# Optimization experiments

Hardware: AMD Instinct MI355X
Metric: run time of the kernel (lower is better)

Reference implementation:

```python
import jax, jax.numpy as jnp
import numpy as np

BATCH, SEQLEN, D_MODEL, D_STATE = 2, 2048, 512, 64
DT_MIN, DT_MAX = 1e-4, 1e-3


def setup_inputs() -> dict:
    key = jax.random.key(0)
    k1, k2, k3, k4 = jax.random.split(key, 4)
    u = jax.random.normal(k1, (BATCH, SEQLEN, D_MODEL), dtype=jnp.float32)
    # real parts of the complex params B, C (imag parts never affect the output)
    B_re = (jax.random.normal(k2, (D_STATE,), dtype=jnp.float32) / np.float32(np.sqrt(D_STATE)))
    C_re = (jax.random.normal(k3, (D_STATE,), dtype=jnp.float32) / np.float32(np.sqrt(D_STATE)))
    log_dt = jax.random.uniform(k4, (D_MODEL,), minval=np.log(DT_MIN), maxval=np.log(DT_MAX)).astype(jnp.float32)
    D = jnp.ones((D_MODEL,), dtype=jnp.float32)
    return {"u": u, "B_re": B_re, "C_re": C_re, "log_dt": log_dt, "D": D}


def reference(u, B_re, C_re, log_dt, D):
    # u: [B, L, H]; B_re/C_re: [N]; log_dt/D: [H]
    N = B_re.shape[0]
    # buffer: log_A = -0.5 * log(1 + n/N), n = 1..N  (A = exp(log_A) in (0,1])
    log_A = -0.5 * jnp.log1p(jnp.arange(1, N + 1, dtype=jnp.float32) / N)
    A = jnp.exp(log_A)                       # [N]
    delta = jnp.exp(log_dt)                  # [H]
    A_d = jnp.exp(delta[:, None] * A[None, :])          # [H, N]
    B_d = (A_d - 1.0) * B_re[None, :] * delta[:, None]  # [H, N]

    Bsz, L, H = u.shape
    x0 = jnp.zeros((Bsz, H, N), dtype=u.dtype)

    def step(x, u_t):                        # x: [B,H,N], u_t: [B,H]
        x = A_d * x + B_d * u_t[..., None]
        y_t = jnp.einsum('bhn,n->bh', x, C_re) + D * u_t
        return x, y_t

    _, ys = jax.lax.scan(step, x0, jnp.swapaxes(u, 0, 1))  # ys: [L,B,H]
    return jnp.swapaxes(ys, 0, 1)                          # [B,L,H]
```

## Files before the change

kernel.cpp:

```cpp
#include <hip/hip_runtime.h>
#include <math.h>


#define BATCH   2
#define SEQLEN  2048
#define DMODEL  512
#define DSTATE  64
#define T_CHUNK 32
#define NCHUNK  64
#define RT      8

__device__ __forceinline__ float A_cont(int n) {
    return rsqrtf(1.0f + (float)(n + 1) * (1.0f / 64.0f));
}

__global__ __launch_bounds__(256) void k_xlocal(const float* __restrict__ u,
                                                const float* __restrict__ B_re,
                                                const float* __restrict__ log_dt,
                                                float* __restrict__ xl) {
    int bid = (int)blockIdx.x;
    int wb  = (bid & 7) * 128 + (bid >> 3);
    int tid = wb * 256 + (int)threadIdx.x;
    int h  = tid & (DMODEL - 1);
    int ng = (tid >> 9) & 3;
    int c  = (tid >> 11) & (NCHUNK - 1);
    int b  = tid >> 17;
    float delta = expf(log_dt[h]);
    float Ad[16], Bd[16], x[16];
    #pragma unroll
    for (int nn = 0; nn < 16; ++nn) {
        int n = ng * 16 + nn;
        float dA = delta * A_cont(n);
        Ad[nn] = expf(dA);
        Bd[nn] = expm1f(dA) * B_re[n] * delta;
        x[nn] = 0.0f;
    }
    const float* up = u + ((size_t)(b * SEQLEN + c * T_CHUNK)) * DMODEL + h;
    #pragma unroll 8
    for (int s = 0; s < T_CHUNK; ++s) {
        float uv = up[(size_t)s * DMODEL];
        #pragma unroll
        for (int nn = 0; nn < 16; ++nn)
            x[nn] = fmaf(Ad[nn], x[nn], Bd[nn] * uv);
    }
    float* xp = xl + ((size_t)((b * NCHUNK + c) * DSTATE + ng * 16)) * DMODEL + h;
    #pragma unroll
    for (int nn = 0; nn < 16; ++nn) xp[(size_t)nn * DMODEL] = x[nn];
}

__global__ __launch_bounds__(256) void k_scanset(const float* __restrict__ B_re,
                                                 const float* __restrict__ C_re,
                                                 const float* __restrict__ log_dt,
                                                 const float* __restrict__ Dp,
                                                 float* __restrict__ xl,
                                                 float* __restrict__ Kbuf,
                                                 float* __restrict__ AdTab,
                                                 float* __restrict__ CpStep) {
    int tid = blockIdx.x * 256 + threadIdx.x;
    {
        int h = tid & (DMODEL - 1);
        int n = (tid >> 9) & (DSTATE - 1);
        int b = tid >> 15;
        float delta = expf(log_dt[h]);
        float ApT = expf(delta * A_cont(n) * (float)T_CHUNK);
        float* base = xl + ((size_t)(b * NCHUNK * DSTATE + n)) * DMODEL + h;
        float v[NCHUNK - 1];
        #pragma unroll
        for (int c = 0; c < NCHUNK - 1; ++c)
            v[c] = base[(size_t)c * DSTATE * DMODEL];
        float s = 0.0f;
        #pragma unroll
        for (int c = 0; c < NCHUNK - 1; ++c) { s = fmaf(ApT, s, v[c]); v[c] = s; }
        #pragma unroll
        for (int c = 0; c < NCHUNK - 1; ++c)
            base[(size_t)c * DSTATE * DMODEL] = v[c];
    }
    if (tid < 32768) {
        int h = tid & (DMODEL - 1);
        int n = tid >> 9;
        float delta = expf(log_dt[h]);
        float Adn = expf(delta * A_cont(n));
        AdTab[n * DMODEL + h] = Adn;
        float sq = Adn * Adn; sq = sq * sq;
        float e8 = sq * sq;
        float p = C_re[n] * Adn;
        #pragma unroll
        for (int i = 0; i < 4; ++i) {
            CpStep[(i * DSTATE + n) * DMODEL + h] = p;
            p *= e8;
        }
        if (n < T_CHUNK) {
            int j = n;
            float acc = (j == 0) ? Dp[h] : 0.0f;
            for (int nn = 0; nn < DSTATE; ++nn) {
                float dAn = delta * A_cont(nn);
                float Bdv = expm1f(dAn) * B_re[nn] * delta;
                acc = fmaf(C_re[nn] * Bdv, expf(dAn * (float)j), acc);
            }
            Kbuf[j * DMODEL + h] = acc;
        }
    }
}

__global__ __launch_bounds__(256) void k_out(const float* __restrict__ u,
                                             const float* __restrict__ Kbuf,
                                             const float* __restrict__ AdTab,
                                             const float* __restrict__ CpStep,
                                             const float* __restrict__ Sbuf,
                                             float* __restrict__ out) {
    int bid = (int)blockIdx.x;
    int wb  = (bid & 7) * 128 + (bid >> 3);
    int tid = wb * 256 + (int)threadIdx.x;
    int h   = tid & (DMODEL - 1);
    int it  = (tid >> 9) & 3;
    int c   = (tid >> 11) & (NCHUNK - 1);
    int b   = tid >> 17;
    int tp0 = it * RT;

    const float* ub = u + ((size_t)(b * SEQLEN + c * T_CHUNK)) * DMODEL + h;
    const float* kb = Kbuf + h;

    float acc[RT];
    #pragma unroll
    for (int i = 0; i < RT; ++i) acc[i] = 0.0f;

    for (int sb = 0; sb < it; ++sb) {
        float ureg[8], krow[15];
        int base = tp0 - sb * 8 - 7;
        #pragma unroll
        for (int q = 0; q < 8; ++q) ureg[q] = ub[(size_t)(sb * 8 + q) * DMODEL];
        #pragma unroll
        for (int j = 0; j < 15; ++j) krow[j] = kb[(size_t)(base + j) * DMODEL];
        #pragma unroll
        for (int q = 0; q < 8; ++q)
            #pragma unroll
            for (int i = 0; i < RT; ++i)
                acc[i] = fmaf(krow[i - q + 7], ureg[q], acc[i]);
    }
    {
        float ureg[8], krow[8];
        #pragma unroll
        for (int q = 0; q < 8; ++q) ureg[q] = ub[(size_t)(tp0 + q) * DMODEL];
        #pragma unroll
        for (int j = 0; j < 8; ++j) krow[j] = kb[(size_t)j * DMODEL];
        #pragma unroll
        for (int q = 0; q < 8; ++q)
            #pragma unroll
            for (int i = 0; i < RT; ++i)
                if (i >= q) acc[i] = fmaf(krow[i - q], ureg[q], acc[i]);
    }
    if (c > 0) {
        const float* sp = Sbuf + ((size_t)((b * NCHUNK + (c - 1)) * DSTATE)) * DMODEL + h;
        const float* ap = AdTab + h;
        const float* cp = CpStep + (size_t)(it * DSTATE) * DMODEL + h;
        #pragma unroll 4
        for (int n = 0; n < DSTATE; ++n) {
            float Sv  = sp[(size_t)n * DMODEL];
            float Adv = ap[(size_t)n * DMODEL];
            float w   = cp[(size_t)n * DMODEL] * Sv;
            acc[0] += w;
            #pragma unroll
            for (int i = 1; i < RT; ++i) { w *= Adv; acc[i] += w; }
        }
    }
    float* ob = out + ((size_t)(b * SEQLEN + c * T_CHUNK + tp0)) * DMODEL + h;
    #pragma unroll
    for (int i = 0; i < RT; ++i)
        __builtin_nontemporal_store(acc[i], &ob[(size_t)i * DMODEL]);
}

extern "C" void kernel_launch(void* const* d_in, const int* in_sizes, int n_in,
                              void* d_out, int out_size, void* d_ws, size_t ws_size,
                              hipStream_t stream) {
    const float* u      = (const float*)d_in[0];
    const float* B_re   = (const float*)d_in[1];
    const float* C_re   = (const float*)d_in[2];
    const float* log_dt = (const float*)d_in[3];
    const float* D      = (const float*)d_in[4];
    float* out = (float*)d_out;
    float* ws  = (float*)d_ws;

    float* Kbuf   = ws;
    float* AdTab  = ws + 16384;
    float* CpStep = ws + 49152;
    float* xl     = ws + 180224;

    k_xlocal <<<1024, 256, 0, stream>>>(u, B_re, log_dt, xl);
    k_scanset<<<256, 256, 0, stream>>>(B_re, C_re, log_dt, D, xl, Kbuf, AdTab, CpStep);
    k_out    <<<1024, 256, 0, stream>>>(u, Kbuf, AdTab, CpStep, xl, out);
}
```

Measured before the change: 112.3 us.

## Replace convolution output with chunk-local recurrence rerun and table precompute

```diff
diff --git a/kernel.cpp b/kernel.cpp
--- a/kernel.cpp
+++ b/kernel.cpp
@@ -8,15 +8,27 @@
 #define DSTATE  64
 #define T_CHUNK 32
 #define NCHUNK  64
-#define RT      8
 
 __device__ __forceinline__ float A_cont(int n) {
     return rsqrtf(1.0f + (float)(n + 1) * (1.0f / 64.0f));
 }
 
+__global__ __launch_bounds__(256) void k_tables(const float* __restrict__ B_re,
+                                                const float* __restrict__ log_dt,
+                                                float* __restrict__ AdT,
+                                                float* __restrict__ BdT) {
+    int tid = blockIdx.x * 256 + threadIdx.x;
+    int h = tid & (DMODEL - 1);
+    int n = tid >> 9;
+    float delta = expf(log_dt[h]);
+    float dA = delta * A_cont(n);
+    AdT[n * DMODEL + h] = expf(dA);
+    BdT[n * DMODEL + h] = expm1f(dA) * B_re[n] * delta;
+}
+
 __global__ __launch_bounds__(256) void k_xlocal(const float* __restrict__ u,
-                                                const float* __restrict__ B_re,
-                                                const float* __restrict__ log_dt,
+                                                const float* __restrict__ AdT,
+                                                const float* __restrict__ BdT,
                                                 float* __restrict__ xl) {
     int bid = (int)blockIdx.x;
     int wb  = (bid & 7) * 128 + (bid >> 3);
@@ -25,14 +37,12 @@
     int ng = (tid >> 9) & 3;
     int c  = (tid >> 11) & (NCHUNK - 1);
     int b  = tid >> 17;
-    float delta = expf(log_dt[h]);
+    int n0 = ng * 16;
     float Ad[16], Bd[16], x[16];
     #pragma unroll
     for (int nn = 0; nn < 16; ++nn) {
-        int n = ng * 16 + nn;
-        float dA = delta * A_cont(n);
-        Ad[nn] = expf(dA);
-        Bd[nn] = expm1f(dA) * B_re[n] * delta;
+        Ad[nn] = AdT[(size_t)(n0 + nn) * DMODEL + h];
+        Bd[nn] = BdT[(size_t)(n0 + nn) * DMODEL + h];
         x[nn] = 0.0f;
     }
     const float* up = u + ((size_t)(b * SEQLEN + c * T_CHUNK)) * DMODEL + h;
@@ -43,130 +53,90 @@
         for (int nn = 0; nn < 16; ++nn)
             x[nn] = fmaf(Ad[nn], x[nn], Bd[nn] * uv);
     }
-    float* xp = xl + ((size_t)((b * NCHUNK + c) * DSTATE + ng * 16)) * DMODEL + h;
+    float* xp = xl + ((size_t)((b * NCHUNK + c) * DSTATE + n0)) * DMODEL + h;
     #pragma unroll
     for (int nn = 0; nn < 16; ++nn) xp[(size_t)nn * DMODEL] = x[nn];
 }
 
-__global__ __launch_bounds__(256) void k_scanset(const float* __restrict__ B_re,
-                                                 const float* __restrict__ C_re,
-                                                 const float* __restrict__ log_dt,
-                                                 const float* __restrict__ Dp,
-                                                 float* __restrict__ xl,
-                                                 float* __restrict__ Kbuf,
-                                                 float* __restrict__ AdTab,
-                                                 float* __restrict__ CpStep) {
+__global__ __launch_bounds__(256) void k_scan(const float* __restrict__ log_dt,
+                                              float* __restrict__ xl) {
     int tid = blockIdx.x * 256 + threadIdx.x;
-    {
-        int h = tid & (DMODEL - 1);
-        int n = (tid >> 9) & (DSTATE - 1);
-        int b = tid >> 15;
-        float delta = expf(log_dt[h]);
-        float ApT = expf(delta * A_cont(n) * (float)T_CHUNK);
-        float* base = xl + ((size_t)(b * NCHUNK * DSTATE + n)) * DMODEL + h;
-        float v[NCHUNK - 1];
-        #pragma unroll
-        for (int c = 0; c < NCHUNK - 1; ++c)
-            v[c] = base[(size_t)c * DSTATE * DMODEL];
-        float s = 0.0f;
-        #pragma unroll
-        for (int c = 0; c < NCHUNK - 1; ++c) { s = fmaf(ApT, s, v[c]); v[c] = s; }
-        #pragma unroll
-        for (int c = 0; c < NCHUNK - 1; ++c)
-            base[(size_t)c * DSTATE * DMODEL] = v[c];
-    }
-    if (tid < 32768) {
-        int h = tid & (DMODEL - 1);
-        int n = tid >> 9;
-        float delta = expf(log_dt[h]);
-        float Adn = expf(delta * A_cont(n));
-        AdTab[n * DMODEL + h] = Adn;
-        float sq = Adn * Adn; sq = sq * sq;
-        float e8 = sq * sq;
-        float p = C_re[n] * Adn;
-        #pragma unroll
-        for (int i = 0; i < 4; ++i) {
-            CpStep[(i * DSTATE + n) * DMODEL + h] = p;
-            p *= e8;
-        }
-        if (n < T_CHUNK) {
-            int j = n;
-            float acc = (j == 0) ? Dp[h] : 0.0f;
-            for (int nn = 0; nn < DSTATE; ++nn) {
-                float dAn = delta * A_cont(nn);
-                float Bdv = expm1f(dAn) * B_re[nn] * delta;
-                acc = fmaf(C_re[nn] * Bdv, expf(dAn * (float)j), acc);
-            }
-            Kbuf[j * DMODEL + h] = acc;
-        }
-    }
+    int h = tid & (DMODEL - 1);
+    int n = (tid >> 9) & (DSTATE - 1);
+    int b = tid >> 15;
+    float delta = expf(log_dt[h]);
+    float ApT = expf(delta * A_cont(n) * (float)T_CHUNK);
+    float* base = xl + ((size_t)(b * NCHUNK * DSTATE + n)) * DMODEL + h;
+    float v[NCHUNK - 1];
+    #pragma unroll
+    for (int c = 0; c < NCHUNK - 1; ++c)
+        v[c] = base[(size_t)c * DSTATE * DMODEL];
+    float s = 0.0f;
+    #pragma unroll
+    for (int c = 0; c < NCHUNK - 1; ++c) { s = fmaf(ApT, s, v[c]); v[c] = s; }
+    #pragma unroll
+    for (int c = 0; c < NCHUNK - 1; ++c)
+        base[(size_t)c * DSTATE * DMODEL] = v[c];
 }
 
-__global__ __launch_bounds__(256) void k_out(const float* __restrict__ u,
-                                             const float* __restrict__ Kbuf,
-                                             const float* __restrict__ AdTab,
-                                             const float* __restrict__ CpStep,
-                                             const float* __restrict__ Sbuf,
-                                             float* __restrict__ out) {
+__global__ __launch_bounds__(256) void k_y(const float* __restrict__ u,
+                                           const float* __restrict__ AdT,
+                                           const float* __restrict__ BdT,
+                                           const float* __restrict__ C_re,
+                                           const float* __restrict__ Dp,
+                                           const float* __restrict__ Sbuf,
+                                           float* __restrict__ out) {
     int bid = (int)blockIdx.x;
     int wb  = (bid & 7) * 128 + (bid >> 3);
     int tid = wb * 256 + (int)threadIdx.x;
-    int h   = tid & (DMODEL - 1);
-    int it  = (tid >> 9) & 3;
-    int c   = (tid >> 11) & (NCHUNK - 1);
-    int b   = tid >> 17;
-    int tp0 = it * RT;
+    int hl = tid & 15;
+    int ng = (tid >> 4) & 3;
+    int hm = (tid >> 6) & 31;
+    int h  = hl | (hm << 4);
+    int c  = (tid >> 11) & (NCHUNK - 1);
+    int b  = tid >> 17;
+    int n0 = ng * 16;
 
-    const float* ub = u + ((size_t)(b * SEQLEN + c * T_CHUNK)) * DMODEL + h;
-    const float* kb = Kbuf + h;
-
-    float acc[RT];
+    float Ad[16], Bd[16], Cw[16], x[16];
     #pragma unroll
-    for (int i = 0; i < RT; ++i) acc[i] = 0.0f;
-
-    for (int sb = 0; sb < it; ++sb) {
-        float ureg[8], krow[15];
-        int base = tp0 - sb * 8 - 7;
-        #pragma unroll
-        for (int q = 0; q < 8; ++q) ureg[q] = ub[(size_t)(sb * 8 + q) * DMODEL];
-        #pragma unroll
-        for (int j = 0; j < 15; ++j) krow[j] = kb[(size_t)(base + j) * DMODEL];
-        #pragma unroll
-        for (int q = 0; q < 8; ++q)
-            #pragma unroll
-            for (int i = 0; i < RT; ++i)
-                acc[i] = fmaf(krow[i - q + 7], ureg[q], acc[i]);
-    }
-    {
-        float ureg[8], krow[8];
-        #pragma unroll
-        for (int q = 0; q < 8; ++q) ureg[q] = ub[(size_t)(tp0 + q) * DMODEL];
-        #pragma unroll
-        for (int j = 0; j < 8; ++j) krow[j] = kb[(size_t)j * DMODEL];
-        #pragma unroll
-        for (int q = 0; q < 8; ++q)
-            #pragma unroll
-            for (int i = 0; i < RT; ++i)
-                if (i >= q) acc[i] = fmaf(krow[i - q], ureg[q], acc[i]);
+    for (int nn = 0; nn < 16; ++nn) {
+        Ad[nn] = AdT[(size_t)(n0 + nn) * DMODEL + h];
+        Bd[nn] = BdT[(size_t)(n0 + nn) * DMODEL + h];
+        Cw[nn] = C_re[n0 + nn];
     }
     if (c > 0) {
-        const float* sp = Sbuf + ((size_t)((b * NCHUNK + (c - 1)) * DSTATE)) * DMODEL + h;
-        const float* ap = AdTab + h;
-        const float* cp = CpStep + (size_t)(it * DSTATE) * DMODEL + h;
-        #pragma unroll 4
-        for (int n = 0; n < DSTATE; ++n) {
-            float Sv  = sp[(size_t)n * DMODEL];
-            float Adv = ap[(size_t)n * DMODEL];
-            float w   = cp[(size_t)n * DMODEL] * Sv;
-            acc[0] += w;
-            #pragma unroll
-            for (int i = 1; i < RT; ++i) { w *= Adv; acc[i] += w; }
+        const float* sp = Sbuf + ((size_t)((b * NCHUNK + (c - 1)) * DSTATE + n0)) * DMODEL + h;
+        #pragma unroll
+        for (int nn = 0; nn < 16; ++nn) x[nn] = sp[(size_t)nn * DMODEL];
+    } else {
+        #pragma unroll
+        for (int nn = 0; nn < 16; ++nn) x[nn] = 0.0f;
+    }
+    float Dv = Dp[h];
+    const float* up = u   + ((size_t)(b * SEQLEN + c * T_CHUNK)) * DMODEL + h;
+    float*       op = out + ((size_t)(b * SEQLEN + c * T_CHUNK)) * DMODEL + h;
+    int store_lane = ((threadIdx.x & 48) == 0);
+
+    #pragma unroll 4
+    for (int t = 0; t < T_CHUNK; ++t) {
+        float uv = up[(size_t)t * DMODEL];
+        #pragma unroll
+        for (int nn = 0; nn < 16; ++nn)
+            x[nn] = fmaf(Ad[nn], x[nn], Bd[nn] * uv);
+        float a0 = 0.0f, a1 = 0.0f, a2 = 0.0f, a3 = 0.0f;
+        #pragma unroll
+        for (int nn = 0; nn < 16; nn += 4) {
+            a0 = fmaf(Cw[nn + 0], x[nn + 0], a0);
+            a1 = fmaf(Cw[nn + 1], x[nn + 1], a1);
+            a2 = fmaf(Cw[nn + 2], x[nn + 2], a2);
+            a3 = fmaf(Cw[nn + 3], x[nn + 3], a3);
         }
+        float acc = (a0 + a1) + (a2 + a3);
+        acc += __shfl_xor(acc, 16);
+        acc += __shfl_xor(acc, 32);
+        if (store_lane)
+            __builtin_nontemporal_store(fmaf(Dv, uv, acc), &op[(size_t)t * DMODEL]);
     }
-    float* ob = out + ((size_t)(b * SEQLEN + c * T_CHUNK + tp0)) * DMODEL + h;
-    #pragma unroll
-    for (int i = 0; i < RT; ++i)
-        __builtin_nontemporal_store(acc[i], &ob[(size_t)i * DMODEL]);
 }
 
 extern "C" void kernel_launch(void* const* d_in, const int* in_sizes, int n_in,
@@ -180,12 +150,12 @@
     float* out = (float*)d_out;
     float* ws  = (float*)d_ws;
 
-    float* Kbuf   = ws;
-    float* AdTab  = ws + 16384;
-    float* CpStep = ws + 49152;
-    float* xl     = ws + 180224;
+    float* AdT = ws;
+    float* BdT = ws + 32768;
+    float* xl  = ws + 65536;
 
-    k_xlocal <<<1024, 256, 0, stream>>>(u, B_re, log_dt, xl);
-    k_scanset<<<256, 256, 0, stream>>>(B_re, C_re, log_dt, D, xl, Kbuf, AdTab, CpStep);
-    k_out    <<<1024, 256, 0, stream>>>(u, Kbuf, AdTab, CpStep, xl, out);
+    k_tables<<<128,  256, 0, stream>>>(B_re, log_dt, AdT, BdT);
+    k_xlocal<<<1024, 256, 0, stream>>>(u, AdT, BdT, xl);
+    k_scan  <<<256,  256, 0, stream>>>(log_dt, xl);
+    k_y     <<<1024, 256, 0, stream>>>(u, AdT, BdT, C_re, D, xl, out);
 }
```

New measurement: 110.1 us. 1.02x faster.
